# Kernel tuning notes

Hardware: AMD Instinct MI355X
Metric: run time of the kernel (lower is better)

## Reference

```python
import jax, jax.numpy as jnp
import numpy as np
import math

N = 100000       # nodes
E = 640000       # edges
VOCAB = 8192
EMB = 96         # node_embedding_dim
SEL = 32         # node_selector_dim
H = EMB + SEL    # hidden_dim = 128
T = 3            # num_edge_types
P = 64           # positional_embedding_dim
MAXPOS = 512     # max_edge_position
ITERS = 6        # ggnn_iterations


def _sinusoidal(max_pos, dim):
    pos = np.arange(max_pos)[:, None].astype(np.float32)
    div = np.exp(np.arange(0, dim, 2).astype(np.float32) * (-math.log(10000.0) / dim))
    pe = np.zeros((max_pos, dim), np.float32)
    pe[:, 0::2] = np.sin(pos * div)
    pe[:, 1::2] = np.cos(pos * div)
    return jnp.asarray(pe)


def setup_inputs() -> dict:
    key = jax.random.key(0)
    ks = jax.random.split(key, 20)
    s = 1.0 / np.sqrt(H).astype(np.float32)
    inp = {
        "x_text_indices": jax.random.randint(ks[0], (N,), 0, VOCAB, dtype=jnp.int32),
        "node_selectors": jax.random.normal(ks[1], (N, SEL), jnp.float32),
        "edge_index": jax.random.randint(ks[2], (2, E), 0, N, dtype=jnp.int32),
        "edge_type": jax.random.randint(ks[3], (E,), 0, T, dtype=jnp.int32),
        "edge_positions": jax.random.randint(ks[4], (E,), 0, MAXPOS + 1, dtype=jnp.int32),
        "emb": (jax.random.normal(ks[5], (VOCAB, EMB), jnp.float32) * 0.02).at[0].set(0.0),  # padding_idx=0
        "pos_enc": _sinusoidal(MAXPOS + 1, P),
        "Wg": jax.random.normal(ks[6], (P, H), jnp.float32) * (1.0 / np.sqrt(P)),
        "bg": jnp.zeros((H,), jnp.float32),
        "Wt": jax.random.normal(ks[7], (T, H, H), jnp.float32) * s,
        "bt": jnp.zeros((T, H), jnp.float32),
        "W_ih": jax.random.normal(ks[8], (3 * H, H), jnp.float32) * s,
        "W_hh": jax.random.normal(ks[9], (3 * H, H), jnp.float32) * s,
        "b_ih": jnp.zeros((3 * H,), jnp.float32),
        "b_hh": jnp.zeros((3 * H,), jnp.float32),
        "W1": jax.random.normal(ks[10], (2 * H, H), jnp.float32) * (1.0 / np.sqrt(2 * H)),
        "b1": jnp.zeros((H,), jnp.float32),
        "W2": jax.random.normal(ks[11], (H, 1), jnp.float32) * s,
        "b2": jnp.zeros((1,), jnp.float32),
    }
    return inp


def _gru_cell(x, h, W_ih, W_hh, b_ih, b_hh):
    # torch.nn.GRUCell math
    gi = x @ W_ih.T + b_ih          # [N, 3H]
    gh = h @ W_hh.T + b_hh          # [N, 3H]
    i_r, i_z, i_n = jnp.split(gi, 3, axis=-1)
    h_r, h_z, h_n = jnp.split(gh, 3, axis=-1)
    r = jax.nn.sigmoid(i_r + h_r)
    z = jax.nn.sigmoid(i_z + h_z)
    n = jnp.tanh(i_n + r * h_n)
    return (1.0 - z) * n + z * h


def reference(x_text_indices, node_selectors, edge_index, edge_type, edge_positions,
              emb, pos_enc, Wg, bg, Wt, bt, W_ih, W_hh, b_ih, b_hh, W1, b1, W2, b2):
    src, dst = edge_index[0], edge_index[1]
    h0 = jnp.concatenate([emb[x_text_indices], node_selectors], axis=-1)  # [N, H]
    pe_e = pos_enc[edge_positions]                                        # [E, P]
    gate = 2.0 * jax.nn.sigmoid(pe_e @ Wg + bg)                           # [E, H]
    cnt = jax.ops.segment_sum(jnp.ones((E,), h0.dtype), dst, num_segments=N)
    denom = jnp.maximum(cnt, 1.0)[:, None]                                # mean-scatter, 0 if no in-edges

    h = h0
    for _ in range(ITERS):
        gx = h[src] * gate                                                # gather + gate [E, H]
        # edge-type routed linear: sum over the one active type per edge
        msg = jnp.zeros_like(gx)
        for t in range(T):
            mask = (edge_type == t)[:, None].astype(gx.dtype)
            msg = msg + mask * (gx @ Wt[t] + bt[t])
        agg = jax.ops.segment_sum(msg, dst, num_segments=N) / denom       # mean aggregation [N, H]
        h = _gru_cell(agg, h, W_ih, W_hh, b_ih, b_hh)

    feats = jnp.concatenate([h, h0], axis=-1)                             # [N, 2H]
    logits = jax.nn.relu(feats @ W1 + b1) @ W2 + b2                       # [N, 1]
    return logits
```

## Files before the change

### kernel.cpp

```cpp
#include <hip/hip_runtime.h>
#include <cstdint>
#include <cstddef>

#define HD 128
#define EMBD 96
#define SELD 32
#define PD 64
#define NPOS 513
#define GITERS 6

typedef _Float16 f16;
typedef __attribute__((ext_vector_type(8))) _Float16 f16x8;
typedef __attribute__((ext_vector_type(4))) _Float16 f16x4;
typedef __attribute__((ext_vector_type(2))) _Float16 f16x2;
typedef __attribute__((ext_vector_type(4))) float f32x4;

__device__ __forceinline__ float sigm(float x) { return 1.0f / (1.0f + __expf(-x)); }


__global__ void k_deg(const int* __restrict__ ei, const int* __restrict__ et,
                      int* __restrict__ deg, int* __restrict__ cnt_t, int E, int N) {
    int e = blockIdx.x * 256 + threadIdx.x;
    if (e < E) {
        int d = ei[E + e];
        atomicAdd(&deg[d], 1);
        atomicAdd(&cnt_t[(size_t)et[e] * N + d], 1);
    }
}

__launch_bounds__(1024)
__global__ void k_scan1(const int* __restrict__ deg, int* __restrict__ rp,
                        int* __restrict__ bsum, int N) {
    __shared__ int sc[1024];
    int t = threadIdx.x;
    int i = blockIdx.x * 1024 + t;
    int v = (i < N) ? deg[i] : 0;
    sc[t] = v;
    __syncthreads();
    for (int off = 1; off < 1024; off <<= 1) {
        int u = (t >= off) ? sc[t - off] : 0;
        __syncthreads();
        sc[t] += u;
        __syncthreads();
    }
    if (i < N) rp[i] = sc[t] - v;
    if (t == 1023) bsum[blockIdx.x] = sc[t];
}

__launch_bounds__(1024)
__global__ void k_scan2(int* __restrict__ bsum, int nb) {
    __shared__ int sc[1024];
    int t = threadIdx.x;
    int v = (t < nb) ? bsum[t] : 0;
    sc[t] = v;
    __syncthreads();
    for (int off = 1; off < 1024; off <<= 1) {
        int u = (t >= off) ? sc[t - off] : 0;
        __syncthreads();
        sc[t] += u;
        __syncthreads();
    }
    if (t < nb) bsum[t] = sc[t] - v;
}

__global__ void k_scan3(const int* __restrict__ rp, const int* __restrict__ bsum,
                        const int* __restrict__ cnt_t, float4* __restrict__ cntp,
                        int4* __restrict__ rp4, int N) {
    int i = blockIdx.x * 256 + threadIdx.x;
    if (i < N) {
        int start = rp[i] + bsum[i >> 10];
        int c0 = cnt_t[i];
        int c1 = cnt_t[(size_t)N + i];
        int c2 = cnt_t[2 * (size_t)N + i];
        rp4[i] = make_int4(start, start + c0, start + c0 + c1, start + c0 + c1 + c2);
        float4 v;
        v.x = (float)c0; v.y = (float)c1; v.z = (float)c2;
        v.w = 1.0f / fmaxf((float)(c0 + c1 + c2), 1.0f);
        cntp[i] = v;
    }
}

__global__ void k_fill(const int* __restrict__ ei, const int* __restrict__ et,
                       const int* __restrict__ ep, const int4* __restrict__ rp4,
                       const int* __restrict__ cnt_t, int* __restrict__ cur3,
                       int2* __restrict__ e2, int E, int N) {
    int e = blockIdx.x * 256 + threadIdx.x;
    if (e < E) {
        int d = ei[E + e];
        int t = et[e];
        int base = rp4[d].x;
        if (t > 0) base += cnt_t[d];
        if (t > 1) base += cnt_t[(size_t)N + d];
        int pos = atomicAdd(&cur3[(size_t)t * N + d], 1);
        e2[base + pos] = make_int2(ei[e], ep[e]);
    }
}

__global__ void k_gate(const float* __restrict__ pe, const float* __restrict__ Wg,
                       const float* __restrict__ bg, f16* __restrict__ gb) {
    int p = blockIdx.x;
    int j = threadIdx.x;
    float acc = bg[j];
    #pragma unroll 8
    for (int k = 0; k < PD; ++k) acc += pe[p * PD + k] * Wg[k * HD + j];
    gb[p * HD + j] = (f16)(2.0f * sigm(acc));
}

__global__ void k_prep(const float* __restrict__ Wt, const float* __restrict__ W1,
                       f16* __restrict__ WtT, f16* __restrict__ W1T) {
    const int SZ = 3 * HD * HD;
    int id = blockIdx.x * 256 + threadIdx.x;
    if (id < SZ) {
        int t = id / (HD * HD), rem = id % (HD * HD);
        int n = rem / HD, k = rem % HD;
        WtT[id] = (f16)Wt[t * HD * HD + k * HD + n];
    } else if (id < SZ + 2 * HD * HD) {
        int rem = id - SZ;
        int n = rem / (2 * HD), k = rem % (2 * HD);
        W1T[rem] = (f16)W1[k * HD + n];
    }
}

__global__ void k_prepW(const float* __restrict__ Wih, const float* __restrict__ Whh,
                        f16* __restrict__ Wcat) {
    int id = blockIdx.x * 256 + threadIdx.x;
    if (id < 512 * 256) {
        int j = id >> 8, k = id & 255;
        float v;
        if (j < 256)      v = (k < 128) ? Wih[j * 128 + k] : Whh[j * 128 + (k - 128)];
        else if (j < 384) v = (k < 128) ? Wih[j * 128 + k] : 0.0f;
        else              v = (k < 128) ? 0.0f : Whh[(j - 128) * 128 + (k - 128)];
        Wcat[id] = (f16)v;
    }
}

__global__ void k_init(const int* __restrict__ xidx, const float* __restrict__ sel,
                       const float* __restrict__ emb, f16* __restrict__ h, int N) {
    int id = blockIdx.x * 256 + threadIdx.x;
    if (id < N * HD) {
        int n = id >> 7, j = id & 127;
        float v = (j < EMBD) ? emb[(size_t)xidx[n] * EMBD + j]
                             : sel[(size_t)n * SELD + (j - EMBD)];
        h[id] = (f16)v;
    }
}

__launch_bounds__(512, 4)
__global__ void k_agg(const int4* __restrict__ rp4, const int2* __restrict__ e2,
                      const f16* __restrict__ h_in, const f16* __restrict__ gb,
                      const f16* __restrict__ WtT, const float* __restrict__ bt,
                      const float4* __restrict__ cntp, f16* __restrict__ agg, int N) {
    __shared__ f16 S[3 * 16 * 136];
    __shared__ f16 aggL[16 * 136];

    int tid = threadIdx.x;
    int wave = tid >> 6, lane = tid & 63;
    int quad = lane >> 4, m = lane & 15;
    int half = lane >> 5, hl = lane & 31;
    int d0 = blockIdx.x * 16;

    {
        int lrow = wave + half * 8;
        int grow = d0 + lrow;
        bool valid = grow < N;
        int4 r4 = rp4[min(grow, N - 1)];
        int es = r4.x, b1 = r4.y, b2 = r4.z, ee = r4.w;
        if (!valid) ee = es;
        int dg = ee - es;
        int dmax = max(dg, __shfl_xor(dg, 32));
        int nb = (__builtin_amdgcn_readfirstlane(dmax) + 7) >> 3;
        int co = hl * 4;

        const f16x4 zf = {0, 0, 0, 0};
        f16x4 accA = zf, accB = zf, accC = zf;
        for (int b = 0; b < nb; ++b) {
            int e0 = es + b * 8;
            int2 ev[8];
            #pragma unroll
            for (int j = 0; j < 8; ++j) {
                int idx = max(min(e0 + j, ee - 1), 0);
                ev[j] = e2[idx];
            }
            f16x4 hv[8], gv[8];
            #pragma unroll
            for (int j = 0; j < 8; ++j) {
                hv[j] = *(const f16x4*)(h_in + (size_t)ev[j].x * HD + co);
                gv[j] = *(const f16x4*)(gb + (size_t)ev[j].y * HD + co);
            }
            #pragma unroll
            for (int j = 0; j < 8; ++j) {
                int eidx = e0 + j;
                f16x4 g0 = (eidx < ee) ? gv[j] : zf;
                accA += hv[j] * g0;
                f16x4 gB = (eidx >= b1) ? g0 : zf;
                accB += hv[j] * gB;
                f16x4 gC = (eidx >= b2) ? g0 : zf;
                accC += hv[j] * gC;
            }
        }
        f16x4 s0 = accA - accB;
        f16x4 s1 = accB - accC;
        *(f16x4*)(S + (0 * 16 + lrow) * 136 + co) = s0;
        *(f16x4*)(S + (1 * 16 + lrow) * 136 + co) = s1;
        *(f16x4*)(S + (2 * 16 + lrow) * 136 + co) = accC;
    }
    __syncthreads();

    {
        int col = wave * 16 + m;
        f32x4 acc = {0.f, 0.f, 0.f, 0.f};
        #pragma unroll
        for (int t = 0; t < 3; ++t)
            #pragma unroll
            for (int c = 0; c < 4; ++c) {
                f16x8 a = *(const f16x8*)(S + (t * 16 + m) * 136 + c * 32 + quad * 8);
                f16x8 b = *(const f16x8*)(WtT + ((size_t)t * HD + col) * HD + c * 32 + quad * 8);
                acc = __builtin_amdgcn_mfma_f32_16x16x32_f16(a, b, acc, 0, 0, 0);
            }
        float bt0 = bt[col], bt1 = bt[HD + col], bt2 = bt[2 * HD + col];
        #pragma unroll
        for (int r = 0; r < 4; ++r) {
            int lr = quad * 4 + r;
            int dd2 = min(d0 + lr, N - 1);
            float4 cp = cntp[dd2];
            float v = (acc[r] + cp.x * bt0 + cp.y * bt1 + cp.z * bt2) * cp.w;
            aggL[lr * 136 + col] = (f16)v;
        }
    }
    __syncthreads();

    {
        int row = tid >> 5, ch = tid & 31;
        if (d0 + row < N) {
            f16x4 v = *(const f16x4*)(aggL + row * 136 + ch * 4);
            *(f16x4*)(agg + (size_t)(d0 + row) * HD + ch * 4) = v;
        }
    }
}

__launch_bounds__(512, 2)
__global__ void k_gru(const f16* __restrict__ agg, const f16* __restrict__ h_in,
                      const f16* __restrict__ Wcat, const float* __restrict__ bih,
                      const float* __restrict__ bhh, f16* __restrict__ h_out, int N) {
    __shared__ f16 AL[64 * 264];

    int tid = threadIdx.x;
    int wave = tid >> 6, lane = tid & 63;
    int quad = lane >> 4, m = lane & 15;
    int d0 = blockIdx.x * 64;

    {
        int rsub = tid >> 5;
        int ch = tid & 31;
        #pragma unroll
        for (int i = 0; i < 4; ++i) {
            int row = i * 16 + rsub;
            int grow = min(d0 + row, N - 1);
            f16x8 v;
            if (ch < 16) v = *(const f16x8*)(agg + (size_t)grow * HD + ch * 8);
            else         v = *(const f16x8*)(h_in + (size_t)grow * HD + (ch - 16) * 8);
            *(f16x8*)(AL + row * 264 + ch * 8) = v;
        }
    }
    __syncthreads();

    f16x8 fa[4][8];
    #pragma unroll
    for (int tau = 0; tau < 4; ++tau)
        #pragma unroll
        for (int c = 0; c < 8; ++c)
            fa[tau][c] = *(const f16x8*)(AL + (tau * 16 + m) * 264 + c * 32 + quad * 8);

    int j = wave * 16 + m;
    f32x4 ar[4], az[4], an[4], ah[4];
    const f32x4 z4 = {0.f, 0.f, 0.f, 0.f};
    #pragma unroll
    for (int tau = 0; tau < 4; ++tau) { ar[tau] = z4; az[tau] = z4; an[tau] = z4; ah[tau] = z4; }

    #pragma unroll
    for (int c = 0; c < 8; ++c) {
        f16x8 br = *(const f16x8*)(Wcat + (size_t)j * 256 + c * 32 + quad * 8);
        f16x8 bz = *(const f16x8*)(Wcat + (size_t)(128 + j) * 256 + c * 32 + quad * 8);
        f16x8 bn = (c < 4)
            ? *(const f16x8*)(Wcat + (size_t)(256 + j) * 256 + c * 32 + quad * 8)
            : *(const f16x8*)(Wcat + (size_t)(384 + j) * 256 + c * 32 + quad * 8);
        #pragma unroll
        for (int tau = 0; tau < 4; ++tau) {
            ar[tau] = __builtin_amdgcn_mfma_f32_16x16x32_f16(fa[tau][c], br, ar[tau], 0, 0, 0);
            az[tau] = __builtin_amdgcn_mfma_f32_16x16x32_f16(fa[tau][c], bz, az[tau], 0, 0, 0);
            if (c < 4) an[tau] = __builtin_amdgcn_mfma_f32_16x16x32_f16(fa[tau][c], bn, an[tau], 0, 0, 0);
            else       ah[tau] = __builtin_amdgcn_mfma_f32_16x16x32_f16(fa[tau][c], bn, ah[tau], 0, 0, 0);
        }
    }

    float b_r  = bih[j] + bhh[j];
    float b_z  = bih[HD + j] + bhh[HD + j];
    float b_in = bih[2 * HD + j];
    float b_hn = bhh[2 * HD + j];
    float hp[4][4];
    #pragma unroll
    for (int tau = 0; tau < 4; ++tau)
        #pragma unroll
        for (int r = 0; r < 4; ++r) {
            int row = tau * 16 + quad * 4 + r;
            float hval = (float)AL[row * 264 + 128 + j];
            float rr = sigm(ar[tau][r] + b_r);
            float zz = sigm(az[tau][r] + b_z);
            float nn = tanhf(an[tau][r] + b_in + rr * (ah[tau][r] + b_hn));
            hp[tau][r] = (1.0f - zz) * nn + zz * hval;
        }
    __syncthreads();

    #pragma unroll
    for (int tau = 0; tau < 4; ++tau)
        #pragma unroll
        for (int r = 0; r < 4; ++r)
            AL[(tau * 16 + quad * 4 + r) * 132 + j] = (f16)hp[tau][r];
    __syncthreads();

    {
        int rsub = tid >> 5, ch = tid & 31;
        #pragma unroll
        for (int i = 0; i < 4; ++i) {
            int row = i * 16 + rsub;
            if (d0 + row < N) {
                f16x4 v = *(const f16x4*)(AL + row * 132 + ch * 4);
                *(f16x4*)(h_out + (size_t)(d0 + row) * HD + ch * 4) = v;
            }
        }
    }
}

__launch_bounds__(256)
__global__ void k_final(const f16* __restrict__ h_f, const int* __restrict__ xidx,
                        const float* __restrict__ sel, const float* __restrict__ emb,
                        const f16* __restrict__ W1T, const float* __restrict__ b1,
                        const float* __restrict__ W2, const float* __restrict__ b2,
                        float* __restrict__ out, int N) {
    __shared__ float red[4][16];
    int tid = threadIdx.x;
    int wave = tid >> 6, lane = tid & 63;
    int quad = lane >> 4, m = lane & 15;
    int row0 = blockIdx.x * 16;
    int arow = min(row0 + m, N - 1);
    int xi = xidx[arow];

    f16x8 fa[8];
    #pragma unroll
    for (int c = 0; c < 4; ++c)
        fa[c] = *(const f16x8*)(h_f + (size_t)arow * HD + c * 32 + quad * 8);
    #pragma unroll
    for (int c = 4; c < 7; ++c) {
        const float* ep = emb + (size_t)xi * EMBD + (c - 4) * 32 + quad * 8;
        #pragma unroll
        for (int jj = 0; jj < 8; ++jj) fa[c][jj] = (f16)ep[jj];
    }
    {
        const float* sp = sel + (size_t)arow * SELD + quad * 8;
        #pragma unroll
        for (int jj = 0; jj < 8; ++jj) fa[7][jj] = (f16)sp[jj];
    }

    f32x4 acc[2];
    const f32x4 z4 = {0.f, 0.f, 0.f, 0.f};
    acc[0] = z4; acc[1] = z4;
    #pragma unroll
    for (int s = 0; s < 2; ++s) {
        int c0 = (wave * 2 + s) * 16;
        #pragma unroll
        for (int c = 0; c < 8; ++c) {
            f16x8 b = *(const f16x8*)(W1T + (size_t)(c0 + m) * (2 * HD) + c * 32 + quad * 8);
            acc[s] = __builtin_amdgcn_mfma_f32_16x16x32_f16(fa[c], b, acc[s], 0, 0, 0);
        }
    }

    float psum[4] = {0.f, 0.f, 0.f, 0.f};
    #pragma unroll
    for (int s = 0; s < 2; ++s) {
        int col = (wave * 2 + s) * 16 + m;
        float b1v = b1[col], w2v = W2[col];
        #pragma unroll
        for (int r = 0; r < 4; ++r)
            psum[r] += fmaxf(acc[s][r] + b1v, 0.0f) * w2v;
    }
    #pragma unroll
    for (int off = 1; off < 16; off <<= 1)
        #pragma unroll
        for (int r = 0; r < 4; ++r) psum[r] += __shfl_xor(psum[r], off);

    if (m == 0) {
        #pragma unroll
        for (int r = 0; r < 4; ++r) red[wave][quad * 4 + r] = psum[r];
    }
    __syncthreads();
    if (tid < 16) {
        int row = row0 + tid;
        if (row < N) out[row] = red[0][tid] + red[1][tid] + red[2][tid] + red[3][tid] + b2[0];
    }
}


extern "C" void kernel_launch(void* const* d_in, const int* in_sizes, int n_in,
                              void* d_out, int out_size, void* d_ws, size_t ws_size,
                              hipStream_t stream) {
    const int*   xidx = (const int*)d_in[0];
    const float* sel  = (const float*)d_in[1];
    const int*   ei   = (const int*)d_in[2];
    const int*   et   = (const int*)d_in[3];
    const int*   ep   = (const int*)d_in[4];
    const float* emb  = (const float*)d_in[5];
    const float* pe   = (const float*)d_in[6];
    const float* Wg   = (const float*)d_in[7];
    const float* bg   = (const float*)d_in[8];
    const float* Wt   = (const float*)d_in[9];
    const float* bt   = (const float*)d_in[10];
    const float* Wih  = (const float*)d_in[11];
    const float* Whh  = (const float*)d_in[12];
    const float* bih  = (const float*)d_in[13];
    const float* bhh  = (const float*)d_in[14];
    const float* W1   = (const float*)d_in[15];
    const float* b1   = (const float*)d_in[16];
    const float* W2   = (const float*)d_in[17];
    const float* b2   = (const float*)d_in[18];

    const int N = in_sizes[0];
    const int E = in_sizes[3];
    const size_t NH = (size_t)N * HD;

    char* p = (char*)d_ws;
    f16*    hbf0  = (f16*)p;    p += NH * 2;
    f16*    hbf1  = (f16*)p;    p += NH * 2;
    f16*    aggb  = (f16*)p;    p += NH * 2;
    f16*    gb    = (f16*)p;    p += (size_t)NPOS * HD * 2;
    f16*    WtT   = (f16*)p;    p += 3 * HD * HD * 2;
    f16*    Wcat  = (f16*)p;    p += 512 * 256 * 2;
    f16*    W1T   = (f16*)p;    p += 2 * HD * HD * 2;
    float4* cntp  = (float4*)p; p += (size_t)N * 16;
    int4*   rp4   = (int4*)p;   p += (size_t)N * 16;
    int* deg    = (int*)p; p += (size_t)N * 4;
    int* cnt_t  = (int*)p; p += 3 * (size_t)N * 4;
    int* rp     = (int*)p; p += (size_t)N * 4;
    int* cur3   = (int*)p; p += 3 * (size_t)N * 4;
    int* bsum   = (int*)p; p += 1024 * 4;
    int2* e2    = (int2*)p;

    hipMemsetAsync(deg, 0, (size_t)N * sizeof(int), stream);
    hipMemsetAsync(cnt_t, 0, 3 * (size_t)N * sizeof(int), stream);
    hipMemsetAsync(cur3, 0, 3 * (size_t)N * sizeof(int), stream);
    k_deg<<<(E + 255) / 256, 256, 0, stream>>>(ei, et, deg, cnt_t, E, N);
    const int nb1 = (N + 1023) / 1024;
    k_scan1<<<nb1, 1024, 0, stream>>>(deg, rp, bsum, N);
    k_scan2<<<1, 1024, 0, stream>>>(bsum, nb1);
    k_scan3<<<(N + 255) / 256, 256, 0, stream>>>(rp, bsum, cnt_t, cntp, rp4, N);
    k_fill<<<(E + 255) / 256, 256, 0, stream>>>(ei, et, ep, rp4, cnt_t, cur3, e2, E, N);
    k_gate<<<NPOS, HD, 0, stream>>>(pe, Wg, bg, gb);
    k_prep<<<(3 * HD * HD + 2 * HD * HD + 255) / 256, 256, 0, stream>>>(Wt, W1, WtT, W1T);
    k_prepW<<<512, 256, 0, stream>>>(Wih, Whh, Wcat);
    k_init<<<(N * HD + 255) / 256, 256, 0, stream>>>(xidx, sel, emb, hbf0, N);

    const int gA = (N + 15) / 16;
    const int gG = (N + 63) / 64;
    const f16* hin = hbf0;
    f16* hout = hbf1;
    for (int it = 0; it < GITERS; ++it) {
        k_agg<<<gA, 512, 0, stream>>>(rp4, e2, hin, gb, WtT, bt, cntp, aggb, N);
        k_gru<<<gG, 512, 0, stream>>>(aggb, hin, Wcat, bih, bhh, hout, N);
        const f16* tmp = hout;
        hout = (f16*)hin;
        hin = tmp;
    }

    const int gF = (N + 15) / 16;
    k_final<<<gF, 256, 0, stream>>>(hin, xidx, sel, emb, W1T, b1, W2, b2, (float*)d_out, N);
}
```

Before: 1.509 ms.

## Drop degree atomics, use fast sigmoid/tanh, and raise GRU occupancy

The separate degree array and its atomics are removed: the scan now sums the three per-type counts, and the fill kernel takes its per-type base offsets from rp4 instead of extra cnt_t loads. The GRU kernel no longer preloads all A fragments into registers. It reads them from LDS inside the MFMA loop and asks for 4 blocks per CU instead of 2, trading extra LDS traffic for lower register pressure and higher occupancy. Sigmoid and tanh now use the hardware reciprocal and an exp-based tanh, which is slightly less accurate.

```diff
diff --git a/kernel.cpp b/kernel.cpp
--- a/kernel.cpp
+++ b/kernel.cpp
@@ -15,26 +15,32 @@
 typedef __attribute__((ext_vector_type(2))) _Float16 f16x2;
 typedef __attribute__((ext_vector_type(4))) float f32x4;
 
-__device__ __forceinline__ float sigm(float x) { return 1.0f / (1.0f + __expf(-x)); }
+__device__ __forceinline__ float sigm(float x) {
+    return __builtin_amdgcn_rcpf(1.0f + __expf(-x));
+}
+__device__ __forceinline__ float tanh_f(float x) {
+    return 2.0f * __builtin_amdgcn_rcpf(1.0f + __expf(-2.0f * x)) - 1.0f;
+}
 
 
 __global__ void k_deg(const int* __restrict__ ei, const int* __restrict__ et,
-                      int* __restrict__ deg, int* __restrict__ cnt_t, int E, int N) {
+                      int* __restrict__ cnt_t, int E, int N) {
     int e = blockIdx.x * 256 + threadIdx.x;
     if (e < E) {
         int d = ei[E + e];
-        atomicAdd(&deg[d], 1);
         atomicAdd(&cnt_t[(size_t)et[e] * N + d], 1);
     }
 }
 
 __launch_bounds__(1024)
-__global__ void k_scan1(const int* __restrict__ deg, int* __restrict__ rp,
+__global__ void k_scan1(const int* __restrict__ cnt_t, int* __restrict__ rp,
                         int* __restrict__ bsum, int N) {
     __shared__ int sc[1024];
     int t = threadIdx.x;
     int i = blockIdx.x * 1024 + t;
-    int v = (i < N) ? deg[i] : 0;
+    int v = 0;
+    if (i < N)
+        v = cnt_t[i] + cnt_t[(size_t)N + i] + cnt_t[2 * (size_t)N + i];
     sc[t] = v;
     __syncthreads();
     for (int off = 1; off < 1024; off <<= 1) {
@@ -82,15 +88,13 @@
 
 __global__ void k_fill(const int* __restrict__ ei, const int* __restrict__ et,
                        const int* __restrict__ ep, const int4* __restrict__ rp4,
-                       const int* __restrict__ cnt_t, int* __restrict__ cur3,
-                       int2* __restrict__ e2, int E, int N) {
+                       int* __restrict__ cur3, int2* __restrict__ e2, int E, int N) {
     int e = blockIdx.x * 256 + threadIdx.x;
     if (e < E) {
         int d = ei[E + e];
         int t = et[e];
-        int base = rp4[d].x;
-        if (t > 0) base += cnt_t[d];
-        if (t > 1) base += cnt_t[(size_t)N + d];
+        int4 r4 = rp4[d];
+        int base = (t == 0) ? r4.x : ((t == 1) ? r4.y : r4.z);
         int pos = atomicAdd(&cur3[(size_t)t * N + d], 1);
         e2[base + pos] = make_int2(ei[e], ep[e]);
     }
@@ -238,7 +242,7 @@
     }
 }
 
-__launch_bounds__(512, 2)
+__launch_bounds__(512, 4)
 __global__ void k_gru(const f16* __restrict__ agg, const f16* __restrict__ h_in,
                       const f16* __restrict__ Wcat, const float* __restrict__ bih,
                       const float* __restrict__ bhh, f16* __restrict__ h_out, int N) {
@@ -264,13 +268,6 @@
     }
     __syncthreads();
 
-    f16x8 fa[4][8];
-    #pragma unroll
-    for (int tau = 0; tau < 4; ++tau)
-        #pragma unroll
-        for (int c = 0; c < 8; ++c)
-            fa[tau][c] = *(const f16x8*)(AL + (tau * 16 + m) * 264 + c * 32 + quad * 8);
-
     int j = wave * 16 + m;
     f32x4 ar[4], az[4], an[4], ah[4];
     const f32x4 z4 = {0.f, 0.f, 0.f, 0.f};
@@ -286,10 +283,11 @@
             : *(const f16x8*)(Wcat + (size_t)(384 + j) * 256 + c * 32 + quad * 8);
         #pragma unroll
         for (int tau = 0; tau < 4; ++tau) {
-            ar[tau] = __builtin_amdgcn_mfma_f32_16x16x32_f16(fa[tau][c], br, ar[tau], 0, 0, 0);
-            az[tau] = __builtin_amdgcn_mfma_f32_16x16x32_f16(fa[tau][c], bz, az[tau], 0, 0, 0);
-            if (c < 4) an[tau] = __builtin_amdgcn_mfma_f32_16x16x32_f16(fa[tau][c], bn, an[tau], 0, 0, 0);
-            else       ah[tau] = __builtin_amdgcn_mfma_f32_16x16x32_f16(fa[tau][c], bn, ah[tau], 0, 0, 0);
+            f16x8 a = *(const f16x8*)(AL + (tau * 16 + m) * 264 + c * 32 + quad * 8);
+            ar[tau] = __builtin_amdgcn_mfma_f32_16x16x32_f16(a, br, ar[tau], 0, 0, 0);
+            az[tau] = __builtin_amdgcn_mfma_f32_16x16x32_f16(a, bz, az[tau], 0, 0, 0);
+            if (c < 4) an[tau] = __builtin_amdgcn_mfma_f32_16x16x32_f16(a, bn, an[tau], 0, 0, 0);
+            else       ah[tau] = __builtin_amdgcn_mfma_f32_16x16x32_f16(a, bn, ah[tau], 0, 0, 0);
         }
     }
 
@@ -306,7 +304,7 @@
             float hval = (float)AL[row * 264 + 128 + j];
             float rr = sigm(ar[tau][r] + b_r);
             float zz = sigm(az[tau][r] + b_z);
-            float nn = tanhf(an[tau][r] + b_in + rr * (ah[tau][r] + b_hn));
+            float nn = tanh_f(an[tau][r] + b_in + rr * (ah[tau][r] + b_hn));
             hp[tau][r] = (1.0f - zz) * nn + zz * hval;
         }
     __syncthreads();
@@ -437,22 +435,20 @@
     f16*    W1T   = (f16*)p;    p += 2 * HD * HD * 2;
     float4* cntp  = (float4*)p; p += (size_t)N * 16;
     int4*   rp4   = (int4*)p;   p += (size_t)N * 16;
-    int* deg    = (int*)p; p += (size_t)N * 4;
     int* cnt_t  = (int*)p; p += 3 * (size_t)N * 4;
     int* rp     = (int*)p; p += (size_t)N * 4;
     int* cur3   = (int*)p; p += 3 * (size_t)N * 4;
     int* bsum   = (int*)p; p += 1024 * 4;
     int2* e2    = (int2*)p;
 
-    hipMemsetAsync(deg, 0, (size_t)N * sizeof(int), stream);
     hipMemsetAsync(cnt_t, 0, 3 * (size_t)N * sizeof(int), stream);
     hipMemsetAsync(cur3, 0, 3 * (size_t)N * sizeof(int), stream);
-    k_deg<<<(E + 255) / 256, 256, 0, stream>>>(ei, et, deg, cnt_t, E, N);
+    k_deg<<<(E + 255) / 256, 256, 0, stream>>>(ei, et, cnt_t, E, N);
     const int nb1 = (N + 1023) / 1024;
-    k_scan1<<<nb1, 1024, 0, stream>>>(deg, rp, bsum, N);
+    k_scan1<<<nb1, 1024, 0, stream>>>(cnt_t, rp, bsum, N);
     k_scan2<<<1, 1024, 0, stream>>>(bsum, nb1);
     k_scan3<<<(N + 255) / 256, 256, 0, stream>>>(rp, bsum, cnt_t, cntp, rp4, N);
-    k_fill<<<(E + 255) / 256, 256, 0, stream>>>(ei, et, ep, rp4, cnt_t, cur3, e2, E, N);
+    k_fill<<<(E + 255) / 256, 256, 0, stream>>>(ei, et, ep, rp4, cur3, e2, E, N);
     k_gate<<<NPOS, HD, 0, stream>>>(pe, Wg, bg, gb);
     k_prep<<<(3 * HD * HD + 2 * HD * HD + 255) / 256, 256, 0, stream>>>(Wt, W1, WtT, W1T);
     k_prepW<<<512, 256, 0, stream>>>(Wih, Whh, Wcat);
```

New measurement: 1.353 ms. 10.4% less time.
